# Performance work log

Measured on AMD Instinct MI355X. Metric: run time of the kernel, lower is better.

Reference implementation:

```python
import jax, jax.numpy as jnp
import numpy as np

B, H, W, DIM, NH = 4, 32, 32, 768, 12
HD = DIM // NH

def setup_inputs() -> dict:
    key = jax.random.key(0)
    ks = jax.random.split(key, 7)
    s = 0.02
    return {
        "x": jax.random.normal(ks[0], (B, H, W, DIM), dtype=jnp.float32),
        "qkv_w": jax.random.normal(ks[1], (3 * DIM, DIM), dtype=jnp.float32) * s,  # torch Linear (out,in)
        "qkv_b": jax.random.normal(ks[2], (3 * DIM,), dtype=jnp.float32) * s,
        "proj_w": jax.random.normal(ks[3], (DIM, DIM), dtype=jnp.float32) * s,
        "proj_b": jax.random.normal(ks[4], (DIM,), dtype=jnp.float32) * s,
        "rel_pos_h": jax.random.normal(ks[5], (2 * H - 1, HD), dtype=jnp.float32) * s,
        "rel_pos_w": jax.random.normal(ks[6], (2 * W - 1, HD), dtype=jnp.float32) * s,
    }

def _get_rel_pos(size, rel_pos):
    # q_size == k_size == size, rel_pos.shape[0] == 2*size-1 -> no interpolation
    idx = jnp.arange(size)[:, None] - jnp.arange(size)[None, :] + (size - 1)
    return rel_pos[idx]  # (size, size, head_dim)

def reference(x, qkv_w, qkv_b, proj_w, proj_b, rel_pos_h, rel_pos_w):
    b, h, w, c = x.shape
    hw = h * w
    hd = c // NH
    scale = hd ** -0.5  # SDPA default scale

    qkv = x @ qkv_w.T + qkv_b                       # (B,H,W,3C)
    qkv = qkv.reshape(b, hw, 3, NH, hd).transpose(2, 0, 3, 1, 4)  # (3,B,nh,HW,hd)
    q, k, v = qkv[0], qkv[1], qkv[2]                # each (B,nh,HW,hd)

    Rh = _get_rel_pos(h, rel_pos_h)                 # (H,H,hd)
    Rw = _get_rel_pos(w, rel_pos_w)                 # (W,W,hd)
    r_q = q.reshape(b, NH, h, w, hd)
    rel_h = jnp.einsum('bnhwc,hkc->bnhwk', r_q, Rh)  # (B,nh,H,W,H)
    rel_w = jnp.einsum('bnhwc,wkc->bnhwk', r_q, Rw)  # (B,nh,H,W,W)
    bias = (rel_h[..., :, None] + rel_w[..., None, :]).reshape(b, NH, hw, hw)

    attn = jnp.einsum('bnqd,bnkd->bnqk', q, k) * scale + bias
    attn = jax.nn.softmax(attn, axis=-1)
    out = jnp.einsum('bnqk,bnkd->bnqd', attn, v)    # (B,nh,HW,hd)
    out = out.reshape(b, NH, h, w, hd).transpose(0, 2, 3, 1, 4).reshape(b, h, w, c)
    return out @ proj_w.T + proj_b
```

## Files before the change

kernel.cpp:

```cpp
#include <hip/hip_runtime.h>
#include <stdint.h>

typedef unsigned short u16;
typedef __attribute__((ext_vector_type(8))) short short8;
typedef __attribute__((ext_vector_type(8))) u16 ushort8;
typedef __attribute__((ext_vector_type(4))) float f32x4;
typedef __attribute__((ext_vector_type(16))) float f32x16;
typedef __attribute__((ext_vector_type(4))) unsigned int uint4v;

#define LOG2E 1.44269504088896f

__device__ __forceinline__ u16 f2bf(float f) {
  unsigned int u = __builtin_bit_cast(unsigned int, f);
  u += 0x7FFF + ((u >> 16) & 1);
  return (u16)(u >> 16);
}
__device__ __forceinline__ unsigned int cvtpk(float a, float b) {
  unsigned int r;
  asm("v_cvt_pk_bf16_f32 %0, %1, %2" : "=v"(r) : "v"(a), "v"(b));
  return r;
}
__device__ __forceinline__ void plswap(unsigned int& a, unsigned int& b) {
  asm("v_permlane32_swap_b32 %0, %1" : "+v"(a), "+v"(b));
}
__device__ __forceinline__ void gload_lds16(const u16* g, u16* l) {
  __builtin_amdgcn_global_load_lds((const __attribute__((address_space(1))) void*)g,
                                   (__attribute__((address_space(3))) void*)l, 16, 0, 0);
}

__global__ __launch_bounds__(256) void cvt_all(
    const float* __restrict__ s0, u16* __restrict__ d0, int n0,
    const float* __restrict__ s1, u16* __restrict__ d1, int n1,
    const float* __restrict__ s2, u16* __restrict__ d2, int n2,
    const float* __restrict__ s3, u16* __restrict__ d3, int n3,
    const float* __restrict__ s4, u16* __restrict__ d4, int n4) {
  const int tid0 = blockIdx.x * 256 + threadIdx.x;
  const int stride = gridDim.x * 256 * 4;
#define CVT_SEG(S, D, N)                                       \
  for (int i = tid0 * 4; i < (N); i += stride) {               \
    float4 v = *(const float4*)((S) + i);                      \
    *(uint2*)((D) + i) = make_uint2(cvtpk(v.x, v.y), cvtpk(v.z, v.w)); \
  }
  CVT_SEG(s0, d0, n0)
  CVT_SEG(s1, d1, n1)
  CVT_SEG(s2, d2, n2)
  CVT_SEG(s3, d3, n3)
  CVT_SEG(s4, d4, n4)
#undef CVT_SEG
}

#define CTS 130
__global__ __launch_bounds__(256) void gemm128q(
    const u16* __restrict__ A, const u16* __restrict__ B,
    const float* __restrict__ bias,
    u16* __restrict__ qo, u16* __restrict__ ko, u16* __restrict__ vto,
    int M, int N, int K) {
  __shared__ u16 smem[4 * 128 * 64];
  const int tid = threadIdx.x;
  const int lane = tid & 63, wave = tid >> 6;
  const int wr = wave >> 1, wc = wave & 1;
  const int l15 = lane & 15, l4 = lane >> 4;
  const int fid = blockIdx.y * gridDim.x + blockIdx.x;
  const int cpx = (gridDim.x * gridDim.y) >> 3;
  const int swz = (fid & 7) * cpx + (fid >> 3);
  const int bxs = swz % gridDim.x, bys = swz / gridDim.x;
  const int bm = bys << 7, bn = bxs << 7;
  f32x4 acc[4][4] = {};
  const int nkt = K >> 6;

#define STAGE(buf, kt)                                                        \
  {                                                                           \
    u16* As_ = smem + (buf) * 16384;                                          \
    u16* Bs_ = As_ + 8192;                                                    \
    const int k0_ = (kt) << 6;                                                \
    _Pragma("unroll") for (int j = 0; j < 4; ++j) {                           \
      const int cbase = j * 256 + wave * 64;                                  \
      const int chunk = cbase + lane;                                         \
      const int row = chunk >> 3;                                             \
      const int co = (((chunk & 7) ^ (row & 7)) << 3);                        \
      gload_lds16(A + (size_t)(bm + row) * K + k0_ + co, As_ + cbase * 8);    \
      gload_lds16(B + (size_t)(bn + row) * K + k0_ + co, Bs_ + cbase * 8);    \
    }                                                                         \
  }

  STAGE(0, 0)
  __syncthreads();
  int cur = 0;
  for (int kt = 0; kt < nkt; ++kt) {
    if (kt + 1 < nkt) STAGE(cur ^ 1, kt + 1)
    const u16* As = smem + cur * 16384;
    const u16* Bs = As + 8192;
    short8 af[2][4], bf[2][4];
#pragma unroll
    for (int kc = 0; kc < 2; ++kc)
#pragma unroll
      for (int i = 0; i < 4; ++i) {
        const int rA = wr * 64 + i * 16 + l15;
        const int rB = wc * 64 + i * 16 + l15;
        af[kc][i] = *(const short8*)((const char*)As +
            (((rA * 64 + kc * 32 + l4 * 8) * 2) ^ ((rA & 7) << 4)));
        bf[kc][i] = *(const short8*)((const char*)Bs +
            (((rB * 64 + kc * 32 + l4 * 8) * 2) ^ ((rB & 7) << 4)));
      }
#pragma unroll
    for (int kc = 0; kc < 2; ++kc)
#pragma unroll
      for (int mi = 0; mi < 4; ++mi)
#pragma unroll
        for (int ni = 0; ni < 4; ++ni)
          acc[mi][ni] = __builtin_amdgcn_mfma_f32_16x16x32_bf16(
              af[kc][mi], bf[kc][ni], acc[mi][ni], 0, 0, 0);
    __syncthreads();
    cur ^= 1;
  }
#undef STAGE

  u16* ct = smem;
  const int which = bn / 768;
  const float sc = (which == 0) ? 0.125f * LOG2E : 1.0f;
#pragma unroll
  for (int ni = 0; ni < 4; ++ni) {
    const int col = wc * 64 + ni * 16 + l15;
    const float bv = bias[bn + col];
#pragma unroll
    for (int mi = 0; mi < 4; ++mi)
#pragma unroll
      for (int j = 0; j < 4; ++j) {
        const int row = wr * 64 + mi * 16 + l4 * 4 + j;
        ct[row * CTS + col] = f2bf((acc[mi][ni][j] + bv) * sc);
      }
  }
  __syncthreads();
  const int nrel = bn - which * 768;
  const int head0 = nrel >> 6;
  const int b = bm >> 10;
  if (which < 2) {
    u16* dst0 = which ? ko : qo;
    const int row = tid >> 1, hp = tid & 1;
    const int head = head0 + hp;
    const int pos = (bm + row) & 1023;
    const u16* s = ct + row * CTS + hp * 64;
    u16* base = dst0 + ((size_t)(b * 12 + head)) * 65536;
    if (which == 0) {
      const int qsub = pos >> 5, lq = pos & 31;
#pragma unroll
      for (int g = 0; g < 8; ++g) {
        const int c = g >> 1, hi = g & 1;
        *(ushort8*)(base + ((qsub * 4 + c) * 64 + hi * 32 + lq) * 8) =
            *(const ushort8*)(s + g * 8);
      }
    } else {
      const int t = pos >> 6, hf = (pos >> 5) & 1, lq = pos & 31;
#pragma unroll
      for (int g = 0; g < 8; ++g) {
        const int c = g >> 1, hi = g & 1;
        *(ushort8*)(base + (((t * 4 + c) * 2 + hf) * 64 + hi * 32 + lq) * 8) =
            *(const ushort8*)(s + g * 8);
      }
    }
  } else {
    const int c = tid >> 1, seg = tid & 1;
    const int head = head0 + (c >> 6), dd = c & 63;
    const int posbase = (bm & 1023) + seg * 64;
    const int t = posbase >> 6;
    const int half = dd >> 5, lqd = dd & 31;
    u16* base = vto + ((size_t)(b * 12 + head)) * 65536;
    const u16* s = ct + (seg * 64) * CTS + c;
#pragma unroll
    for (int g = 0; g < 8; ++g) {
      ushort8 o;
#pragma unroll
      for (int e = 0; e < 8; ++e) o[e] = s[(g * 8 + e) * CTS];
      *(ushort8*)(base + (((t * 4 + (g >> 1)) * 2 + half) * 64 + (g & 1) * 32 + lqd) * 8) = o;
    }
  }
}

__global__ __launch_bounds__(256) void gemm64(
    const u16* __restrict__ A, const u16* __restrict__ B,
    const float* __restrict__ bias, float* __restrict__ fout,
    int M, int N, int K) {
  __shared__ u16 smem[2 * 8192];
  const int tid = threadIdx.x;
  const int lane = tid & 63, wave = tid >> 6;
  const int wr = wave >> 1, wc = wave & 1;
  const int l15 = lane & 15, l4 = lane >> 4;
  const int fid = blockIdx.y * gridDim.x + blockIdx.x;
  const int cpx = (gridDim.x * gridDim.y) >> 3;
  const int swz = (fid & 7) * cpx + (fid >> 3);
  const int bxs = swz % gridDim.x, bys = swz / gridDim.x;
  const int bm = bys << 6, bn = bxs << 6;
  f32x4 acc[2][2] = {};
  const int nkt = K >> 6;

#define STAGE64(buf, kt)                                                      \
  {                                                                           \
    u16* As_ = smem + (buf) * 8192;                                           \
    u16* Bs_ = As_ + 4096;                                                    \
    const int k0_ = (kt) << 6;                                                \
    _Pragma("unroll") for (int j = 0; j < 2; ++j) {                           \
      const int cbase = j * 256 + wave * 64;                                  \
      const int chunk = cbase + lane;                                         \
      const int row = chunk >> 3;                                             \
      const int co = (((chunk & 7) ^ (row & 7)) << 3);                        \
      gload_lds16(A + (size_t)(bm + row) * K + k0_ + co, As_ + cbase * 8);    \
      gload_lds16(B + (size_t)(bn + row) * K + k0_ + co, Bs_ + cbase * 8);    \
    }                                                                         \
  }

  STAGE64(0, 0)
  __syncthreads();
  int cur = 0;
  for (int kt = 0; kt < nkt; ++kt) {
    if (kt + 1 < nkt) STAGE64(cur ^ 1, kt + 1)
    const u16* As = smem + cur * 8192;
    const u16* Bs = As + 4096;
    short8 af[2][2], bf[2][2];
#pragma unroll
    for (int kc = 0; kc < 2; ++kc)
#pragma unroll
      for (int i = 0; i < 2; ++i) {
        const int rA = wr * 32 + i * 16 + l15;
        const int rB = wc * 32 + i * 16 + l15;
        af[kc][i] = *(const short8*)((const char*)As +
            (((rA * 64 + kc * 32 + l4 * 8) * 2) ^ ((rA & 7) << 4)));
        bf[kc][i] = *(const short8*)((const char*)Bs +
            (((rB * 64 + kc * 32 + l4 * 8) * 2) ^ ((rB & 7) << 4)));
      }
#pragma unroll
    for (int kc = 0; kc < 2; ++kc)
#pragma unroll
      for (int mi = 0; mi < 2; ++mi)
#pragma unroll
        for (int ni = 0; ni < 2; ++ni)
          acc[mi][ni] = __builtin_amdgcn_mfma_f32_16x16x32_bf16(
              af[kc][mi], bf[kc][ni], acc[mi][ni], 0, 0, 0);
    __syncthreads();
    cur ^= 1;
  }
#undef STAGE64

#pragma unroll
  for (int ni = 0; ni < 2; ++ni) {
    const int col = wc * 32 + ni * 16 + l15;
    const float bv = bias[bn + col];
#pragma unroll
    for (int mi = 0; mi < 2; ++mi)
#pragma unroll
      for (int j = 0; j < 4; ++j) {
        const int row = wr * 32 + mi * 16 + l4 * 4 + j;
        fout[(size_t)(bm + row) * N + bn + col] = acc[mi][ni][j] + bv;
      }
  }
}

__global__ __launch_bounds__(64) void rel_kernel(
    const u16* __restrict__ pq, const u16* __restrict__ th,
    float* __restrict__ rhp) {
  const int bh = blockIdx.x, h = blockIdx.y;
  const int lane = threadIdx.x & 63, lq = lane & 31, hi = lane >> 5;
  short8 qf[4];
#pragma unroll
  for (int c = 0; c < 4; ++c)
    qf[c] = *(const short8*)(pq + (size_t)bh * 65536 + ((h * 4 + c) * 64 + lane) * 8);
  const int tr = h - lq + 31;
  f32x16 acc{};
#pragma unroll
  for (int c = 0; c < 4; ++c) {
    short8 bfr = *(const short8*)(th + tr * 64 + c * 16 + hi * 8);
    acc = __builtin_amdgcn_mfma_f32_32x32x16_bf16(qf[c], bfr, acc, 0, 0, 0);
  }
  float* O = rhp + (size_t)bh * 32768 + lq * 1024 + h * 32;
#pragma unroll
  for (int r = 0; r < 16; ++r) {
    const int w = (r & 3) + 8 * (r >> 2) + 4 * hi;
    O[w] = acc[r] * 8.0f;
  }
}

__global__ __launch_bounds__(256) void attn_kernel(
    const u16* __restrict__ pq, const u16* __restrict__ pk,
    const u16* __restrict__ pv, const float* __restrict__ rhp,
    const u16* __restrict__ tw, u16* __restrict__ aout) {
  const int bh = blockIdx.x, qt = blockIdx.y;
  const int tid = threadIdx.x, lane = tid & 63, wave = tid >> 6;
  const int wq = wave >> 1, wk = wave & 1;
  const int lq = lane & 31, hi = lane >> 5;
  const int q0 = qt * 64 + wq * 32;
  const u16* Qb = pq + (size_t)bh * 65536;
  const u16* Kb = pk + (size_t)bh * 65536;
  const u16* Vb = pv + (size_t)bh * 65536;
  const float* RH = rhp + (size_t)bh * 32768;
  __shared__ float part[2][2][64][17];
  __shared__ float lsums[2][2][32];
  __shared__ float pd_lds[2][64][32];
  const int qg = q0 + lq;
  const int qsub = qt * 2 + wq;
  short8 qf[4];
#pragma unroll
  for (int c = 0; c < 4; ++c)
    qf[c] = *(const short8*)(Qb + ((qsub * 4 + c) * 64 + lane) * 8);
  short8 kf[2][8];
  {
    const int t0 = wk * 8;
#pragma unroll
    for (int c = 0; c < 4; ++c) {
      kf[0][c]     = *(const short8*)(Kb + (((t0 * 4 + c) * 2 + 0) * 64 + lane) * 8);
      kf[0][4 + c] = *(const short8*)(Kb + (((t0 * 4 + c) * 2 + 1) * 64 + lane) * 8);
    }
  }
  if (wk == 0) {
    f32x16 pa{}, pb{};
    const int trB = (lq == 31) ? 62 : 32 + lq;
#pragma unroll
    for (int c = 0; c < 4; ++c) {
      short8 ta = *(const short8*)(tw + (lq * 64 + c * 16 + hi * 8));
      short8 tb = *(const short8*)(tw + (trB * 64 + c * 16 + hi * 8));
      pa = __builtin_amdgcn_mfma_f32_32x32x16_bf16(ta, qf[c], pa, 0, 0, 0);
      pb = __builtin_amdgcn_mfma_f32_32x32x16_bf16(tb, qf[c], pb, 0, 0, 0);
    }
#pragma unroll
    for (int r = 0; r < 16; ++r) {
      const int j = (r & 3) + 8 * (r >> 2) + 4 * hi;
      pd_lds[wq][j][lq] = pa[r] * 8.0f;
      pd_lds[wq][32 + j][lq] = pb[r] * 8.0f;
    }
  }
  float rhv[16];
#pragma unroll
  for (int i = 0; i < 16; ++i)
    rhv[i] = RH[(16 * wk + i) * 1024 + qg];
  __syncthreads();
  float rw[16];
#pragma unroll
  for (int r = 0; r < 16; ++r)
    rw[r] = pd_lds[wq][lq + 31 - ((r & 3) + 8 * (r >> 2) + 4 * hi)][lq];
  f32x16 o0{}, o1{};
  float lsum = 0.f;
#pragma unroll
  for (int t = 0; t < 8; ++t) {
    const int tt = wk * 8 + t;
    const int cur = t & 1, nxt = cur ^ 1;
    short8 vb0[4], vb1[4];
#pragma unroll
    for (int cc = 0; cc < 4; ++cc) {
      vb0[cc] = *(const short8*)(Vb + (((tt * 4 + cc) * 2 + 0) * 64 + lane) * 8);
      vb1[cc] = *(const short8*)(Vb + (((tt * 4 + cc) * 2 + 1) * 64 + lane) * 8);
    }
    if (t < 7) {
      const int tn = tt + 1;
#pragma unroll
      for (int c = 0; c < 4; ++c) {
        kf[nxt][c]     = *(const short8*)(Kb + (((tn * 4 + c) * 2 + 0) * 64 + lane) * 8);
        kf[nxt][4 + c] = *(const short8*)(Kb + (((tn * 4 + c) * 2 + 1) * 64 + lane) * 8);
      }
    }
    f32x16 s0{}, s1{};
    __builtin_amdgcn_s_setprio(1);
#pragma unroll
    for (int c = 0; c < 4; ++c) {
      s0 = __builtin_amdgcn_mfma_f32_32x32x16_bf16(kf[cur][c], qf[c], s0, 0, 0, 0);
      s1 = __builtin_amdgcn_mfma_f32_32x32x16_bf16(kf[cur][4 + c], qf[c], s1, 0, 0, 0);
    }
    __builtin_amdgcn_s_setprio(0);
    const float rh0 = rhv[2 * t], rh1 = rhv[2 * t + 1];
#pragma unroll
    for (int r = 0; r < 16; ++r) {
      s0[r] = exp2f(s0[r] + (rh0 + rw[r]));
      s1[r] = exp2f(s1[r] + (rh1 + rw[r]));
    }
#pragma unroll
    for (int r = 0; r < 16; ++r) lsum += s0[r] + s1[r];
    unsigned int pw[16];
#pragma unroll
    for (int j = 0; j < 8; ++j) pw[j] = cvtpk(s0[2 * j], s0[2 * j + 1]);
#pragma unroll
    for (int j = 0; j < 8; ++j) pw[8 + j] = cvtpk(s1[2 * j], s1[2 * j + 1]);
    plswap(pw[0], pw[2]);  plswap(pw[1], pw[3]);
    plswap(pw[4], pw[6]);  plswap(pw[5], pw[7]);
    plswap(pw[8], pw[10]); plswap(pw[9], pw[11]);
    plswap(pw[12], pw[14]); plswap(pw[13], pw[15]);
    __builtin_amdgcn_s_setprio(1);
#pragma unroll
    for (int cc = 0; cc < 4; ++cc) {
      uint4v w4 = {pw[cc * 4 + 0], pw[cc * 4 + 1], pw[cc * 4 + 2], pw[cc * 4 + 3]};
      short8 pa = __builtin_bit_cast(short8, w4);
      o0 = __builtin_amdgcn_mfma_f32_32x32x16_bf16(pa, vb0[cc], o0, 0, 0, 0);
      o1 = __builtin_amdgcn_mfma_f32_32x32x16_bf16(pa, vb1[cc], o1, 0, 0, 0);
    }
    __builtin_amdgcn_s_setprio(0);
  }
  lsum += __shfl_xor(lsum, 32, 64);
  if (hi == 0) lsums[wq][wk][lq] = lsum;
#pragma unroll
  for (int r = 0; r < 16; ++r)
    part[wq][wk][lane][r] = wk ? o0[r] : o1[r];
  __syncthreads();
  const int b = bh / 12, head = bh - b * 12;
  u16* outp = aout + (size_t)b * 1024 * 768 + head * 64 + wk * 32;
#pragma unroll
  for (int r = 0; r < 16; ++r) {
    const int qr = (r & 3) + 8 * (r >> 2) + 4 * hi;
    const float inv = 1.0f / (lsums[wq][0][qr] + lsums[wq][1][qr]);
    const float own = wk ? o1[r] : o0[r];
    const float val = own + part[wq][wk ^ 1][lane][r];
    outp[(size_t)(q0 + qr) * 768 + lq] = f2bf(val * inv);
  }
}

extern "C" void kernel_launch(void* const* d_in, const int* in_sizes, int n_in,
                              void* d_out, int out_size, void* d_ws, size_t ws_size,
                              hipStream_t stream) {
  const float* x = (const float*)d_in[0];
  const float* qkv_w = (const float*)d_in[1];
  const float* qkv_b = (const float*)d_in[2];
  const float* proj_w = (const float*)d_in[3];
  const float* proj_b = (const float*)d_in[4];
  const float* rph = (const float*)d_in[5];
  const float* rpw = (const float*)d_in[6];
  float* out = (float*)d_out;
  char* ws = (char*)d_ws;
  u16* xb     = (u16*)(ws + 0);
  u16* wqkv   = (u16*)(ws + 6291456);
  u16* wproj  = (u16*)(ws + 9830400);
  u16* pq     = (u16*)(ws + 11010048);
  u16* pk     = (u16*)(ws + 17301504);
  u16* pv     = (u16*)(ws + 23592960);
  float* rhp  = (float*)(ws + 29884416);
  u16* aout   = (u16*)(ws + 42467328);
  u16* rphb   = (u16*)(ws + 48758784);
  u16* rpwb   = (u16*)(ws + 48766848);

  cvt_all<<<1024, 256, 0, stream>>>(x, xb, 3145728, qkv_w, wqkv, 1769472,
                                    proj_w, wproj, 589824, rph, rphb, 4032,
                                    rpw, rpwb, 4032);
  gemm128q<<<dim3(18, 32), 256, 0, stream>>>(xb, wqkv, qkv_b, pq, pk, pv,
                                             4096, 2304, 768);
  rel_kernel<<<dim3(48, 32), 64, 0, stream>>>(pq, rphb, rhp);
  attn_kernel<<<dim3(48, 16), 256, 0, stream>>>(pq, pk, pv, rhp, rpwb, aout);
  gemm64<<<dim3(12, 64), 256, 0, stream>>>(aout, wproj, proj_b, out,
                                           4096, 768, 768);
}
```

Baseline: 81.61 us.

## Fuse relative-height bias computation into attention kernel and alias shared memory

Removes the separate rel_kernel launch and its fp32 global buffer of rel_h values. Instead, the otherwise idle wk==1 waves compute the height bias with MFMA into shared memory, in parallel with the wk==0 waves computing the width bias. The shared buffers for biases and partial outputs are aliased into one raw array, which needs an extra barrier. This saves one launch and a 6MB round trip through global memory, at the cost of slightly more per-block prologue work.

```diff
diff --git a/kernel.cpp b/kernel.cpp
--- a/kernel.cpp
+++ b/kernel.cpp
@@ -254,33 +254,9 @@
   }
 }
 
-__global__ __launch_bounds__(64) void rel_kernel(
-    const u16* __restrict__ pq, const u16* __restrict__ th,
-    float* __restrict__ rhp) {
-  const int bh = blockIdx.x, h = blockIdx.y;
-  const int lane = threadIdx.x & 63, lq = lane & 31, hi = lane >> 5;
-  short8 qf[4];
-#pragma unroll
-  for (int c = 0; c < 4; ++c)
-    qf[c] = *(const short8*)(pq + (size_t)bh * 65536 + ((h * 4 + c) * 64 + lane) * 8);
-  const int tr = h - lq + 31;
-  f32x16 acc{};
-#pragma unroll
-  for (int c = 0; c < 4; ++c) {
-    short8 bfr = *(const short8*)(th + tr * 64 + c * 16 + hi * 8);
-    acc = __builtin_amdgcn_mfma_f32_32x32x16_bf16(qf[c], bfr, acc, 0, 0, 0);
-  }
-  float* O = rhp + (size_t)bh * 32768 + lq * 1024 + h * 32;
-#pragma unroll
-  for (int r = 0; r < 16; ++r) {
-    const int w = (r & 3) + 8 * (r >> 2) + 4 * hi;
-    O[w] = acc[r] * 8.0f;
-  }
-}
-
 __global__ __launch_bounds__(256) void attn_kernel(
     const u16* __restrict__ pq, const u16* __restrict__ pk,
-    const u16* __restrict__ pv, const float* __restrict__ rhp,
+    const u16* __restrict__ pv, const u16* __restrict__ th,
     const u16* __restrict__ tw, u16* __restrict__ aout) {
   const int bh = blockIdx.x, qt = blockIdx.y;
   const int tid = threadIdx.x, lane = tid & 63, wave = tid >> 6;
@@ -290,11 +266,11 @@
   const u16* Qb = pq + (size_t)bh * 65536;
   const u16* Kb = pk + (size_t)bh * 65536;
   const u16* Vb = pv + (size_t)bh * 65536;
-  const float* RH = rhp + (size_t)bh * 32768;
-  __shared__ float part[2][2][64][17];
   __shared__ float lsums[2][2][32];
-  __shared__ float pd_lds[2][64][32];
-  const int qg = q0 + lq;
+  __shared__ char shraw[24576];
+  float* pd = (float*)shraw;
+  float* rhl = (float*)(shraw + 16384);
+  float* part = (float*)shraw;
   const int qsub = qt * 2 + wq;
   short8 qf[4];
 #pragma unroll
@@ -322,19 +298,33 @@
 #pragma unroll
     for (int r = 0; r < 16; ++r) {
       const int j = (r & 3) + 8 * (r >> 2) + 4 * hi;
-      pd_lds[wq][j][lq] = pa[r] * 8.0f;
-      pd_lds[wq][32 + j][lq] = pb[r] * 8.0f;
-    }
-  }
+      pd[(wq * 64 + j) * 32 + lq] = pa[r] * 8.0f;
+      pd[(wq * 64 + 32 + j) * 32 + lq] = pb[r] * 8.0f;
+    }
+  } else {
+    f32x16 rha{};
+    const int trh = qsub - lq + 31;
+#pragma unroll
+    for (int c = 0; c < 4; ++c) {
+      short8 ta = *(const short8*)(th + (trh * 64 + c * 16 + hi * 8));
+      rha = __builtin_amdgcn_mfma_f32_32x32x16_bf16(ta, qf[c], rha, 0, 0, 0);
+    }
+#pragma unroll
+    for (int r = 0; r < 16; ++r) {
+      const int kh = (r & 3) + 8 * (r >> 2) + 4 * hi;
+      rhl[(wq * 32 + kh) * 32 + lq] = rha[r] * 8.0f;
+    }
+  }
+  __syncthreads();
   float rhv[16];
 #pragma unroll
   for (int i = 0; i < 16; ++i)
-    rhv[i] = RH[(16 * wk + i) * 1024 + qg];
-  __syncthreads();
+    rhv[i] = rhl[(wq * 32 + 16 * wk + i) * 32 + lq];
   float rw[16];
 #pragma unroll
   for (int r = 0; r < 16; ++r)
-    rw[r] = pd_lds[wq][lq + 31 - ((r & 3) + 8 * (r >> 2) + 4 * hi)][lq];
+    rw[r] = pd[(wq * 64 + lq + 31 - ((r & 3) + 8 * (r >> 2) + 4 * hi)) * 32 + lq];
+  __syncthreads();
   f32x16 o0{}, o1{};
   float lsum = 0.f;
 #pragma unroll
@@ -394,7 +384,7 @@
   if (hi == 0) lsums[wq][wk][lq] = lsum;
 #pragma unroll
   for (int r = 0; r < 16; ++r)
-    part[wq][wk][lane][r] = wk ? o0[r] : o1[r];
+    part[((wq * 2 + wk) * 64 + lane) * 17 + r] = wk ? o0[r] : o1[r];
   __syncthreads();
   const int b = bh / 12, head = bh - b * 12;
   u16* outp = aout + (size_t)b * 1024 * 768 + head * 64 + wk * 32;
@@ -403,7 +393,7 @@
     const int qr = (r & 3) + 8 * (r >> 2) + 4 * hi;
     const float inv = 1.0f / (lsums[wq][0][qr] + lsums[wq][1][qr]);
     const float own = wk ? o1[r] : o0[r];
-    const float val = own + part[wq][wk ^ 1][lane][r];
+    const float val = own + part[((wq * 2 + (wk ^ 1)) * 64 + lane) * 17 + r];
     outp[(size_t)(q0 + qr) * 768 + lq] = f2bf(val * inv);
   }
 }
@@ -426,7 +416,6 @@
   u16* pq     = (u16*)(ws + 11010048);
   u16* pk     = (u16*)(ws + 17301504);
   u16* pv     = (u16*)(ws + 23592960);
-  float* rhp  = (float*)(ws + 29884416);
   u16* aout   = (u16*)(ws + 42467328);
   u16* rphb   = (u16*)(ws + 48758784);
   u16* rpwb   = (u16*)(ws + 48766848);
@@ -436,8 +425,7 @@
                                     rpw, rpwb, 4032);
   gemm128q<<<dim3(18, 32), 256, 0, stream>>>(xb, wqkv, qkv_b, pq, pk, pv,
                                              4096, 2304, 768);
-  rel_kernel<<<dim3(48, 32), 64, 0, stream>>>(pq, rphb, rhp);
-  attn_kernel<<<dim3(48, 16), 256, 0, stream>>>(pq, pk, pv, rhp, rpwb, aout);
+  attn_kernel<<<dim3(48, 16), 256, 0, stream>>>(pq, pk, pv, rphb, rpwb, aout);
   gemm64<<<dim3(12, 64), 256, 0, stream>>>(aout, wproj, proj_b, out,
                                            4096, 768, 768);
 }
```

Result: faster. 78.23 us (-4.1%).
